# Kernel optimization log

Measured on AMD Instinct MI355X. Metric: run time of the kernel, lower is better.

The kernel has to match this reference:

```python
import jax, jax.numpy as jnp
import numpy as np

L, B, E = 512, 4, 256
SCALE = 0.05  # keep sigmoid in a non-saturated range


def setup_inputs() -> dict:
    key = jax.random.key(0)
    ks = jax.random.split(key, 6)
    return {
        "emb": jax.random.normal(ks[0], (L, B, E), dtype=jnp.float32),
        "w1": jax.random.normal(ks[1], (E, E), dtype=jnp.float32) * SCALE,
        "w2": jax.random.normal(ks[2], (E, E), dtype=jnp.float32) * SCALE,
        "w3": jax.random.normal(ks[3], (E, E), dtype=jnp.float32) * SCALE,
        "b3": jax.random.normal(ks[4], (E,), dtype=jnp.float32) * SCALE,
        "w0": jax.random.normal(ks[5], (E,), dtype=jnp.float32) * SCALE,
    }


def reference(emb, w1, w2, w3, b3, w0):
    # emb: (L, B, E). torch Linear computes x @ W.T (+ b).
    Lq = emb.shape[0]
    u = jnp.einsum('lbe,fe->lbf', emb, w1)                      # w1(x_i), per key i
    q = jnp.einsum('lbe,fe->lbf', emb, w2)                      # w2(x_t), per query t
    c = jnp.einsum('lbe,fe->lbf', jnp.cumsum(emb, axis=0), w3) + b3  # w3(cumsum up to t)
    # gate[t, i, b, e] = sigmoid(u[i] + q[t] + c[t]); additive score via w0
    gate = jax.nn.sigmoid(u[None, :, :, :] + (q + c)[:, None, :, :])  # (L, L, B, E)
    scores = jnp.einsum('tibe,e->tib', gate, w0)                # (L, L, B)
    causal = jnp.tril(jnp.ones((Lq, Lq), dtype=emb.dtype))      # i <= t
    scores = scores * causal[:, :, None]
    # m_a[t] = sum_{i<=t} a_i * x_i
    return jnp.einsum('tib,ibe->tbe', scores, emb)              # (L, B, E)
```

## Files before the change

kernel.cpp:

```cpp
#include <hip/hip_runtime.h>
#include <hip/hip_bf16.h>

#define L_  512
#define B_  4
#define E_  256
#define TT  8
#define TI  64

typedef unsigned short u16;
#define NLOG2E (-1.44269504f)

__device__ __forceinline__ float bflo(unsigned u) { return __uint_as_float(u << 16); }
__device__ __forceinline__ float bfhi(unsigned u) { return __uint_as_float(u & 0xffff0000u); }

__device__ __forceinline__ unsigned pack_bf2(float x, float y) {
  __hip_bfloat162 h = __float22bfloat162_rn(make_float2(x, y));
  return *reinterpret_cast<unsigned*>(&h);
}

__device__ __forceinline__ float sigs(float xs) {
  float e = __builtin_amdgcn_exp2f(xs);
  return __builtin_amdgcn_rcpf(1.0f + e);
}

__global__ __launch_bounds__(256) void gemm3_k(
    const float* __restrict__ A,
    const float* __restrict__ w1, const float* __restrict__ w2, const float* __restrict__ w3,
    float* __restrict__ o1, float* __restrict__ o2, float* __restrict__ o3) {
  __shared__ float As[64 * 32], Ws[64 * 32];
  const int tid = threadIdx.x, tx = tid & 15, ty = tid >> 4;
  const int r0 = blockIdx.x * 64, f0 = blockIdx.y * 64, z = blockIdx.z;
  const float* W = (z == 0) ? w1 : (z == 1) ? w2 : w3;
  float* O = (z == 0) ? o1 : (z == 1) ? o2 : o3;
  float acc[4][4] = {};
  for (int kb = 0; kb < 256; kb += 32) {
    for (int j = 0; j < 2; ++j) {
      int idx = j * 256 + tid;
      int r = idx >> 3, g = idx & 7;
      float4 av = *(const float4*)(A + (size_t)(r0 + r) * E_ + kb + g * 4);
      float4 wv = *(const float4*)(W + (size_t)(f0 + r) * E_ + kb + g * 4);
      int gs = g ^ ((r >> 2) & 7);
      *(float4*)(As + r * 32 + gs * 4) = av;
      *(float4*)(Ws + r * 32 + gs * 4) = wv;
    }
    __syncthreads();
#pragma unroll
    for (int g = 0; g < 8; ++g) {
      float4 a[4], w[4];
#pragma unroll
      for (int i = 0; i < 4; ++i) {
        int r = ty * 4 + i;
        a[i] = *(const float4*)(As + r * 32 + (g ^ ((r >> 2) & 7)) * 4);
        int f = tx * 4 + i;
        w[i] = *(const float4*)(Ws + f * 32 + (g ^ ((f >> 2) & 7)) * 4);
      }
#pragma unroll
      for (int i = 0; i < 4; ++i)
#pragma unroll
        for (int j = 0; j < 4; ++j)
          acc[i][j] += a[i].x * w[j].x + a[i].y * w[j].y + a[i].z * w[j].z + a[i].w * w[j].w;
    }
    __syncthreads();
  }
  const float scl = (z == 0) ? NLOG2E : 1.0f;
#pragma unroll
  for (int i = 0; i < 4; ++i) {
    float4 v = make_float4(acc[i][0] * scl, acc[i][1] * scl, acc[i][2] * scl, acc[i][3] * scl);
    *(float4*)(O + (size_t)(r0 + ty * 4 + i) * E_ + f0 + tx * 4) = v;
  }
}

__global__ __launch_bounds__(256) void scan_k(
    const float* __restrict__ v3, float* __restrict__ q2qc, const float* __restrict__ b3g) {
  const int bc = blockIdx.x;
  const int cg = threadIdx.x & 3;
  const int rk = threadIdx.x >> 2;
  const int C = bc * 16 + cg * 4;
  __shared__ float4 s_p[64][4];
  float4 part = {0.f, 0.f, 0.f, 0.f};
  for (int l = rk * 8; l < rk * 8 + 8; ++l) {
    float4 v = *(const float4*)(v3 + (size_t)l * 1024 + C);
    part.x += v.x; part.y += v.y; part.z += v.z; part.w += v.w;
  }
  s_p[rk][cg] = part;
  __syncthreads();
  float4 run = {0.f, 0.f, 0.f, 0.f};
  for (int k = 0; k < rk; ++k) {
    float4 p = s_p[k][cg];
    run.x += p.x; run.y += p.y; run.z += p.z; run.w += p.w;
  }
  const int e = C & 255;
  float4 bb = *(const float4*)(b3g + e);
  for (int l = rk * 8; l < rk * 8 + 8; ++l) {
    size_t o = (size_t)l * 1024 + C;
    float4 v = *(const float4*)(v3 + o);
    run.x += v.x; run.y += v.y; run.z += v.z; run.w += v.w;
    float4 q = *(const float4*)(q2qc + o);
    float4 r;
    r.x = NLOG2E * (q.x + bb.x + run.x);
    r.y = NLOG2E * (q.y + bb.y + run.y);
    r.z = NLOG2E * (q.z + bb.z + run.z);
    r.w = NLOG2E * (q.w + bb.w + run.w);
    *(float4*)(q2qc + o) = r;
  }
}

__global__ __launch_bounds__(256) void attn_main_k(
    const float* __restrict__ emb, const float* __restrict__ U,
    const float* __restrict__ QC, const float* __restrict__ w0g,
    float* __restrict__ out) {
  const int tt = blockIdx.x, ic = blockIdx.y, b = blockIdx.z;
  const int t0 = tt * TT, i0 = ic * TI;
  if (i0 > t0) return;

  __shared__ u16 tile[TI * 264];
  __shared__ float s_s[TT][TI];
  const int tid = threadIdx.x, wave = tid >> 6, lane = tid & 63;

  {
    const float* src = U + ((size_t)i0 * B_ + b) * E_ + lane * 4;
#pragma unroll
    for (int c = 0; c < 16; ++c) {
      int r = c * 4 + wave;
      float4 v = *(const float4*)(src + (size_t)r * (B_ * E_));
      *(uint2*)(tile + r * 264 + lane * 4) =
          make_uint2(pack_bf2(v.x, v.y), pack_bf2(v.z, v.w));
    }
  }
  __syncthreads();

  const int tA = t0 + wave * 2, tB = tA + 1;
  {
    int rA = __builtin_amdgcn_readfirstlane(tA * B_ + b);
    int rB = __builtin_amdgcn_readfirstlane(tB * B_ + b);
    const float* qA = QC + (size_t)rA * E_;
    const float* qB = QC + (size_t)rB * E_;
    const u16* urow = tile + lane * 264;
    float a0 = 0.f, a1 = 0.f, a2 = 0.f, a3 = 0.f;
    float c0 = 0.f, c1 = 0.f, c2 = 0.f, c3 = 0.f;
#pragma unroll 4
    for (int g = 0; g < 32; ++g) {
      uint4 raw = *(const uint4*)(urow + g * 8);
      float4 z0 = *(const float4*)(w0g + g * 8);
      float4 z1 = *(const float4*)(w0g + g * 8 + 4);
      float4 qa0 = *(const float4*)(qA + g * 8);
      float4 qa1 = *(const float4*)(qA + g * 8 + 4);
      float4 qb0 = *(const float4*)(qB + g * 8);
      float4 qb1 = *(const float4*)(qB + g * 8 + 4);
      float u0 = bflo(raw.x), u1 = bfhi(raw.x), u2 = bflo(raw.y), u3 = bfhi(raw.y);
      float u4 = bflo(raw.z), u5 = bfhi(raw.z), u6 = bflo(raw.w), u7 = bfhi(raw.w);
      a0 += z0.x * sigs(u0 + qa0.x); a1 += z0.y * sigs(u1 + qa0.y);
      a2 += z0.z * sigs(u2 + qa0.z); a3 += z0.w * sigs(u3 + qa0.w);
      a0 += z1.x * sigs(u4 + qa1.x); a1 += z1.y * sigs(u5 + qa1.y);
      a2 += z1.z * sigs(u6 + qa1.z); a3 += z1.w * sigs(u7 + qa1.w);
      c0 += z0.x * sigs(u0 + qb0.x); c1 += z0.y * sigs(u1 + qb0.y);
      c2 += z0.z * sigs(u2 + qb0.z); c3 += z0.w * sigs(u3 + qb0.w);
      c0 += z1.x * sigs(u4 + qb1.x); c1 += z1.y * sigs(u5 + qb1.y);
      c2 += z1.z * sigs(u6 + qb1.z); c3 += z1.w * sigs(u7 + qb1.w);
    }
    float sA = (a0 + a1) + (a2 + a3), sB = (c0 + c1) + (c2 + c3);
    int i = i0 + lane;
    s_s[wave * 2][lane]     = (i <= tA) ? sA : 0.f;
    s_s[wave * 2 + 1][lane] = (i <= tB) ? sB : 0.f;
  }
  __syncthreads();

  {
    const float* embp = emb + ((size_t)i0 * B_ + b) * E_ + lane * 4;
    const float* sAv = s_s[wave * 2];
    const float* sBv = s_s[wave * 2 + 1];
    int nI = min(TI, tB - i0 + 1);
    nI = (nI + 3) & ~3;
    float4 o0 = {0.f, 0.f, 0.f, 0.f}, o1 = {0.f, 0.f, 0.f, 0.f};
    for (int i = 0; i < nI; i += 4) {
#pragma unroll
      for (int k = 0; k < 4; ++k) {
        float4 r = *(const float4*)(embp + (size_t)(i + k) * (B_ * E_));
        float s0 = sAv[i + k], s1 = sBv[i + k];
        o0.x += s0 * r.x; o0.y += s0 * r.y; o0.z += s0 * r.z; o0.w += s0 * r.w;
        o1.x += s1 * r.x; o1.y += s1 * r.y; o1.z += s1 * r.z; o1.w += s1 * r.w;
      }
    }
    float* opA = out + ((size_t)tA * B_ + b) * E_ + lane * 4;
    float* opB = out + ((size_t)tB * B_ + b) * E_ + lane * 4;
    atomicAdd(opA + 0, o0.x); atomicAdd(opA + 1, o0.y);
    atomicAdd(opA + 2, o0.z); atomicAdd(opA + 3, o0.w);
    atomicAdd(opB + 0, o1.x); atomicAdd(opB + 1, o1.y);
    atomicAdd(opB + 2, o1.z); atomicAdd(opB + 3, o1.w);
  }
}

extern "C" void kernel_launch(void* const* d_in, const int* in_sizes, int n_in,
                              void* d_out, int out_size, void* d_ws, size_t ws_size,
                              hipStream_t stream) {
  const float* emb = (const float*)d_in[0];
  const float* w1  = (const float*)d_in[1];
  const float* w2  = (const float*)d_in[2];
  const float* w3  = (const float*)d_in[3];
  const float* b3  = (const float*)d_in[4];
  const float* w0  = (const float*)d_in[5];
  float* out = (float*)d_out;

  float* U  = (float*)d_ws;
  float* Q2 = U + 524288;
  float* V3 = Q2 + 524288;

  hipMemsetAsync(out, 0, (size_t)524288 * sizeof(float), stream);
  gemm3_k<<<dim3(32, 4, 3), 256, 0, stream>>>(emb, w1, w2, w3, U, Q2, V3);
  scan_k<<<dim3(64), 256, 0, stream>>>(V3, Q2, b3);
  attn_main_k<<<dim3(L_ / TT, L_ / TI, B_), 256, 0, stream>>>(emb, U, Q2, w0, out);
}
```

Measured before the change: 152.6 us.

## Scan embeddings before GEMM, fuse q and c projections, retile attention kernel

The cumulative sum now runs on the embeddings first, and the q and c projections are computed as one K=512 GEMM over [emb, cumsum(emb)] with [w2, w3]. The bias and the exp2 scaling are folded into that GEMM's epilogue, which removes the separate V3 buffer and the scan pass over the GEMM output. Zeroing the output moves into the prescan kernel, replacing the memset launch. The attention kernel changes to 16 query rows by 32 key rows with 512 threads, each half-wave computing one query row, to raise parallelism and reduce wasted work on the causal triangle.

New measurement: 204.6 us. 1.34x slower.

```diff
diff --git a/kernel.cpp b/kernel.cpp
--- a/kernel.cpp
+++ b/kernel.cpp
@@ -4,8 +4,8 @@
 #define L_  512
 #define B_  4
 #define E_  256
-#define TT  8
-#define TI  64
+#define TT  16
+#define TI  32
 
 typedef unsigned short u16;
 #define NLOG2E (-1.44269504f)
@@ -23,63 +23,16 @@
   return __builtin_amdgcn_rcpf(1.0f + e);
 }
 
-__global__ __launch_bounds__(256) void gemm3_k(
-    const float* __restrict__ A,
-    const float* __restrict__ w1, const float* __restrict__ w2, const float* __restrict__ w3,
-    float* __restrict__ o1, float* __restrict__ o2, float* __restrict__ o3) {
-  __shared__ float As[64 * 32], Ws[64 * 32];
-  const int tid = threadIdx.x, tx = tid & 15, ty = tid >> 4;
-  const int r0 = blockIdx.x * 64, f0 = blockIdx.y * 64, z = blockIdx.z;
-  const float* W = (z == 0) ? w1 : (z == 1) ? w2 : w3;
-  float* O = (z == 0) ? o1 : (z == 1) ? o2 : o3;
-  float acc[4][4] = {};
-  for (int kb = 0; kb < 256; kb += 32) {
-    for (int j = 0; j < 2; ++j) {
-      int idx = j * 256 + tid;
-      int r = idx >> 3, g = idx & 7;
-      float4 av = *(const float4*)(A + (size_t)(r0 + r) * E_ + kb + g * 4);
-      float4 wv = *(const float4*)(W + (size_t)(f0 + r) * E_ + kb + g * 4);
-      int gs = g ^ ((r >> 2) & 7);
-      *(float4*)(As + r * 32 + gs * 4) = av;
-      *(float4*)(Ws + r * 32 + gs * 4) = wv;
-    }
-    __syncthreads();
-#pragma unroll
-    for (int g = 0; g < 8; ++g) {
-      float4 a[4], w[4];
-#pragma unroll
-      for (int i = 0; i < 4; ++i) {
-        int r = ty * 4 + i;
-        a[i] = *(const float4*)(As + r * 32 + (g ^ ((r >> 2) & 7)) * 4);
-        int f = tx * 4 + i;
-        w[i] = *(const float4*)(Ws + f * 32 + (g ^ ((f >> 2) & 7)) * 4);
-      }
-#pragma unroll
-      for (int i = 0; i < 4; ++i)
-#pragma unroll
-        for (int j = 0; j < 4; ++j)
-          acc[i][j] += a[i].x * w[j].x + a[i].y * w[j].y + a[i].z * w[j].z + a[i].w * w[j].w;
-    }
-    __syncthreads();
-  }
-  const float scl = (z == 0) ? NLOG2E : 1.0f;
-#pragma unroll
-  for (int i = 0; i < 4; ++i) {
-    float4 v = make_float4(acc[i][0] * scl, acc[i][1] * scl, acc[i][2] * scl, acc[i][3] * scl);
-    *(float4*)(O + (size_t)(r0 + ty * 4 + i) * E_ + f0 + tx * 4) = v;
-  }
-}
-
-__global__ __launch_bounds__(256) void scan_k(
-    const float* __restrict__ v3, float* __restrict__ q2qc, const float* __restrict__ b3g) {
+__global__ __launch_bounds__(256) void prescan_k(
+    const float* __restrict__ emb, float* __restrict__ CE, float* __restrict__ out0) {
   const int bc = blockIdx.x;
-  const int cg = threadIdx.x & 3;
-  const int rk = threadIdx.x >> 2;
-  const int C = bc * 16 + cg * 4;
-  __shared__ float4 s_p[64][4];
+  const int cg = threadIdx.x & 1;
+  const int rk = threadIdx.x >> 1;
+  const int col = bc * 8 + cg * 4;
+  __shared__ float4 s_p[128][2];
   float4 part = {0.f, 0.f, 0.f, 0.f};
-  for (int l = rk * 8; l < rk * 8 + 8; ++l) {
-    float4 v = *(const float4*)(v3 + (size_t)l * 1024 + C);
+  for (int l = rk * 4; l < rk * 4 + 4; ++l) {
+    float4 v = *(const float4*)(emb + (size_t)l * 1024 + col);
     part.x += v.x; part.y += v.y; part.z += v.z; part.w += v.w;
   }
   s_p[rk][cg] = part;
@@ -89,39 +42,129 @@
     float4 p = s_p[k][cg];
     run.x += p.x; run.y += p.y; run.z += p.z; run.w += p.w;
   }
-  const int e = C & 255;
-  float4 bb = *(const float4*)(b3g + e);
-  for (int l = rk * 8; l < rk * 8 + 8; ++l) {
-    size_t o = (size_t)l * 1024 + C;
-    float4 v = *(const float4*)(v3 + o);
+  for (int l = rk * 4; l < rk * 4 + 4; ++l) {
+    size_t o = (size_t)l * 1024 + col;
+    float4 v = *(const float4*)(emb + o);
     run.x += v.x; run.y += v.y; run.z += v.z; run.w += v.w;
-    float4 q = *(const float4*)(q2qc + o);
-    float4 r;
-    r.x = NLOG2E * (q.x + bb.x + run.x);
-    r.y = NLOG2E * (q.y + bb.y + run.y);
-    r.z = NLOG2E * (q.z + bb.z + run.z);
-    r.w = NLOG2E * (q.w + bb.w + run.w);
-    *(float4*)(q2qc + o) = r;
-  }
-}
-
-__global__ __launch_bounds__(256) void attn_main_k(
+    *(float4*)(CE + o) = run;
+  }
+  const float4 z = {0.f, 0.f, 0.f, 0.f};
+  float* op = out0 + ((size_t)bc * 256 + threadIdx.x) * 16;
+#pragma unroll
+  for (int j = 0; j < 4; ++j) *(float4*)(op + j * 4) = z;
+}
+
+__global__ __launch_bounds__(256) void gemm_k(
+    const float* __restrict__ emb, const float* __restrict__ CE,
+    const float* __restrict__ w1, const float* __restrict__ w2, const float* __restrict__ w3,
+    const float* __restrict__ b3, float* __restrict__ U, float* __restrict__ QC) {
+  __shared__ float As[64 * 32], Ws[64 * 32];
+  const int tid = threadIdx.x, tx = tid & 15, ty = tid >> 4;
+  const int bx = blockIdx.x;
+  if (bx < 128) {
+    const int r0 = (bx >> 2) * 64, f0 = (bx & 3) * 64;
+    float acc[4][4] = {};
+    for (int kb = 0; kb < 256; kb += 32) {
+      for (int j = 0; j < 2; ++j) {
+        int idx = j * 256 + tid;
+        int r = idx >> 3, g = idx & 7;
+        int gs = g ^ ((r >> 2) & 7);
+        *(float4*)(As + r * 32 + gs * 4) = *(const float4*)(emb + (size_t)(r0 + r) * E_ + kb + g * 4);
+        *(float4*)(Ws + r * 32 + gs * 4) = *(const float4*)(w1 + (size_t)(f0 + r) * E_ + kb + g * 4);
+      }
+      __syncthreads();
+#pragma unroll
+      for (int g = 0; g < 8; ++g) {
+        float4 a[4], w[4];
+#pragma unroll
+        for (int i = 0; i < 4; ++i) {
+          int r = ty * 4 + i;
+          a[i] = *(const float4*)(As + r * 32 + (g ^ ((r >> 2) & 7)) * 4);
+          int f = tx * 4 + i;
+          w[i] = *(const float4*)(Ws + f * 32 + (g ^ ((f >> 2) & 7)) * 4);
+        }
+#pragma unroll
+        for (int i = 0; i < 4; ++i)
+#pragma unroll
+          for (int j = 0; j < 4; ++j)
+            acc[i][j] += a[i].x * w[j].x + a[i].y * w[j].y + a[i].z * w[j].z + a[i].w * w[j].w;
+      }
+      __syncthreads();
+    }
+#pragma unroll
+    for (int i = 0; i < 4; ++i) {
+      float4 v = make_float4(acc[i][0] * NLOG2E, acc[i][1] * NLOG2E,
+                             acc[i][2] * NLOG2E, acc[i][3] * NLOG2E);
+      *(float4*)(U + (size_t)(r0 + ty * 4 + i) * E_ + f0 + tx * 4) = v;
+    }
+  } else {
+    const int y = bx - 128;
+    const int r0 = (y >> 2) * 32, f0 = (y & 3) * 64;
+    float acc[2][4] = {};
+    for (int kb16 = 0; kb16 < 16; ++kb16) {
+      const float* A = (kb16 < 8) ? emb : CE;
+      const float* W = (kb16 < 8) ? w2 : w3;
+      const int kk = (kb16 & 7) * 32;
+      {
+        int r = tid >> 3, g = tid & 7;
+        int gs = g ^ ((r >> 2) & 7);
+        *(float4*)(As + r * 32 + gs * 4) = *(const float4*)(A + (size_t)(r0 + r) * E_ + kk + g * 4);
+      }
+      for (int j = 0; j < 2; ++j) {
+        int idx = j * 256 + tid;
+        int fr = idx >> 3, g = idx & 7;
+        int gs = g ^ ((fr >> 2) & 7);
+        *(float4*)(Ws + fr * 32 + gs * 4) = *(const float4*)(W + (size_t)(f0 + fr) * E_ + kk + g * 4);
+      }
+      __syncthreads();
+#pragma unroll
+      for (int g = 0; g < 8; ++g) {
+        float4 a[2], w[4];
+#pragma unroll
+        for (int i = 0; i < 2; ++i) {
+          int r = ty * 2 + i;
+          a[i] = *(const float4*)(As + r * 32 + (g ^ ((r >> 2) & 7)) * 4);
+        }
+#pragma unroll
+        for (int j = 0; j < 4; ++j) {
+          int f = tx * 4 + j;
+          w[j] = *(const float4*)(Ws + f * 32 + (g ^ ((f >> 2) & 7)) * 4);
+        }
+#pragma unroll
+        for (int i = 0; i < 2; ++i)
+#pragma unroll
+          for (int j = 0; j < 4; ++j)
+            acc[i][j] += a[i].x * w[j].x + a[i].y * w[j].y + a[i].z * w[j].z + a[i].w * w[j].w;
+      }
+      __syncthreads();
+    }
+    float4 bb = *(const float4*)(b3 + f0 + tx * 4);
+#pragma unroll
+    for (int i = 0; i < 2; ++i) {
+      float4 v = make_float4(NLOG2E * (acc[i][0] + bb.x), NLOG2E * (acc[i][1] + bb.y),
+                             NLOG2E * (acc[i][2] + bb.z), NLOG2E * (acc[i][3] + bb.w));
+      *(float4*)(QC + (size_t)(r0 + ty * 2 + i) * E_ + f0 + tx * 4) = v;
+    }
+  }
+}
+
+__global__ __launch_bounds__(512, 8) void attn_main_k(
     const float* __restrict__ emb, const float* __restrict__ U,
     const float* __restrict__ QC, const float* __restrict__ w0g,
     float* __restrict__ out) {
-  const int tt = blockIdx.x, ic = blockIdx.y, b = blockIdx.z;
-  const int t0 = tt * TT, i0 = ic * TI;
+  const int t0 = blockIdx.x * TT, i0 = blockIdx.y * TI, b = blockIdx.z;
   if (i0 > t0) return;
 
   __shared__ u16 tile[TI * 264];
   __shared__ float s_s[TT][TI];
   const int tid = threadIdx.x, wave = tid >> 6, lane = tid & 63;
+  const int il = lane & 31, eh = lane >> 5;
 
   {
     const float* src = U + ((size_t)i0 * B_ + b) * E_ + lane * 4;
 #pragma unroll
-    for (int c = 0; c < 16; ++c) {
-      int r = c * 4 + wave;
+    for (int c = 0; c < 4; ++c) {
+      int r = c * 8 + wave;
       float4 v = *(const float4*)(src + (size_t)r * (B_ * E_));
       *(uint2*)(tile + r * 264 + lane * 4) =
           make_uint2(pack_bf2(v.x, v.y), pack_bf2(v.z, v.w));
@@ -129,43 +172,31 @@
   }
   __syncthreads();
 
-  const int tA = t0 + wave * 2, tB = tA + 1;
   {
-    int rA = __builtin_amdgcn_readfirstlane(tA * B_ + b);
-    int rB = __builtin_amdgcn_readfirstlane(tB * B_ + b);
-    const float* qA = QC + (size_t)rA * E_;
-    const float* qB = QC + (size_t)rB * E_;
-    const u16* urow = tile + lane * 264;
+    const int t = t0 + wave * 2 + eh;
+    const float* qrow = QC + ((size_t)t * B_ + b) * E_;
+    const u16* urow = tile + il * 264;
     float a0 = 0.f, a1 = 0.f, a2 = 0.f, a3 = 0.f;
-    float c0 = 0.f, c1 = 0.f, c2 = 0.f, c3 = 0.f;
 #pragma unroll 4
     for (int g = 0; g < 32; ++g) {
       uint4 raw = *(const uint4*)(urow + g * 8);
+      float4 q0 = *(const float4*)(qrow + g * 8);
+      float4 q1 = *(const float4*)(qrow + g * 8 + 4);
       float4 z0 = *(const float4*)(w0g + g * 8);
       float4 z1 = *(const float4*)(w0g + g * 8 + 4);
-      float4 qa0 = *(const float4*)(qA + g * 8);
-      float4 qa1 = *(const float4*)(qA + g * 8 + 4);
-      float4 qb0 = *(const float4*)(qB + g * 8);
-      float4 qb1 = *(const float4*)(qB + g * 8 + 4);
-      float u0 = bflo(raw.x), u1 = bfhi(raw.x), u2 = bflo(raw.y), u3 = bfhi(raw.y);
-      float u4 = bflo(raw.z), u5 = bfhi(raw.z), u6 = bflo(raw.w), u7 = bfhi(raw.w);
-      a0 += z0.x * sigs(u0 + qa0.x); a1 += z0.y * sigs(u1 + qa0.y);
-      a2 += z0.z * sigs(u2 + qa0.z); a3 += z0.w * sigs(u3 + qa0.w);
-      a0 += z1.x * sigs(u4 + qa1.x); a1 += z1.y * sigs(u5 + qa1.y);
-      a2 += z1.z * sigs(u6 + qa1.z); a3 += z1.w * sigs(u7 + qa1.w);
-      c0 += z0.x * sigs(u0 + qb0.x); c1 += z0.y * sigs(u1 + qb0.y);
-      c2 += z0.z * sigs(u2 + qb0.z); c3 += z0.w * sigs(u3 + qb0.w);
-      c0 += z1.x * sigs(u4 + qb1.x); c1 += z1.y * sigs(u5 + qb1.y);
-      c2 += z1.z * sigs(u6 + qb1.z); c3 += z1.w * sigs(u7 + qb1.w);
-    }
-    float sA = (a0 + a1) + (a2 + a3), sB = (c0 + c1) + (c2 + c3);
-    int i = i0 + lane;
-    s_s[wave * 2][lane]     = (i <= tA) ? sA : 0.f;
-    s_s[wave * 2 + 1][lane] = (i <= tB) ? sB : 0.f;
+      a0 += z0.x * sigs(bflo(raw.x) + q0.x); a1 += z0.y * sigs(bfhi(raw.x) + q0.y);
+      a2 += z0.z * sigs(bflo(raw.y) + q0.z); a3 += z0.w * sigs(bfhi(raw.y) + q0.w);
+      a0 += z1.x * sigs(bflo(raw.z) + q1.x); a1 += z1.y * sigs(bfhi(raw.z) + q1.y);
+      a2 += z1.z * sigs(bflo(raw.w) + q1.z); a3 += z1.w * sigs(bfhi(raw.w) + q1.w);
+    }
+    float s = (a0 + a1) + (a2 + a3);
+    if (i0 + il > t) s = 0.f;
+    s_s[0][wave * 64 + lane] = s;
   }
   __syncthreads();
 
   {
+    const int tA = t0 + wave * 2, tB = tA + 1;
     const float* embp = emb + ((size_t)i0 * B_ + b) * E_ + lane * 4;
     const float* sAv = s_s[wave * 2];
     const float* sBv = s_s[wave * 2 + 1];
@@ -174,11 +205,11 @@
     float4 o0 = {0.f, 0.f, 0.f, 0.f}, o1 = {0.f, 0.f, 0.f, 0.f};
     for (int i = 0; i < nI; i += 4) {
 #pragma unroll
-      for (int k = 0; k < 4; ++k) {
-        float4 r = *(const float4*)(embp + (size_t)(i + k) * (B_ * E_));
-        float s0 = sAv[i + k], s1 = sBv[i + k];
-        o0.x += s0 * r.x; o0.y += s0 * r.y; o0.z += s0 * r.z; o0.w += s0 * r.w;
-        o1.x += s1 * r.x; o1.y += s1 * r.y; o1.z += s1 * r.z; o1.w += s1 * r.w;
+      for (int k2 = 0; k2 < 4; ++k2) {
+        float4 r = *(const float4*)(embp + (size_t)(i + k2) * (B_ * E_));
+        float sa = sAv[i + k2], sb = sBv[i + k2];
+        o0.x += sa * r.x; o0.y += sa * r.y; o0.z += sa * r.z; o0.w += sa * r.w;
+        o1.x += sb * r.x; o1.y += sb * r.y; o1.z += sb * r.z; o1.w += sb * r.w;
       }
     }
     float* opA = out + ((size_t)tA * B_ + b) * E_ + lane * 4;
@@ -201,12 +232,11 @@
   const float* w0  = (const float*)d_in[5];
   float* out = (float*)d_out;
 
-  float* U  = (float*)d_ws;
-  float* Q2 = U + 524288;
-  float* V3 = Q2 + 524288;
-
-  hipMemsetAsync(out, 0, (size_t)524288 * sizeof(float), stream);
-  gemm3_k<<<dim3(32, 4, 3), 256, 0, stream>>>(emb, w1, w2, w3, U, Q2, V3);
-  scan_k<<<dim3(64), 256, 0, stream>>>(V3, Q2, b3);
-  attn_main_k<<<dim3(L_ / TT, L_ / TI, B_), 256, 0, stream>>>(emb, U, Q2, w0, out);
-}
+  float* CE = (float*)d_ws;
+  float* U  = CE + 524288;
+  float* QC = U + 524288;
+
+  prescan_k<<<dim3(128), 256, 0, stream>>>(emb, CE, out);
+  gemm_k<<<dim3(384), 256, 0, stream>>>(emb, CE, w1, w2, w3, b3, U, QC);
+  attn_main_k<<<dim3(L_ / TT, L_ / TI, B_), 512, 0, stream>>>(emb, U, QC, w0, out);
+}
```
